# Optimization experiments

Measured on AMD Instinct MI355X. Metric: run time of the kernel, lower is better.

## Reference

```python
import jax, jax.numpy as jnp
import numpy as np
from jax import lax

B, S, T = 256, 2048, 64


def setup_inputs() -> dict:
    key = jax.random.key(0)
    k1, k2, k3 = jax.random.split(key, 3)
    emissions = jax.random.normal(k1, (B, S, T), dtype=jnp.float32)
    tags = jax.random.randint(k2, (B, S), 0, T, dtype=jnp.int64)
    mask = jnp.ones((B, S), dtype=bool)
    # learned parameter: transitions ~ U(-0.1, 0.1) per reset_parameters
    transitions = jax.random.uniform(k3, (T, T), dtype=jnp.float32, minval=-0.1, maxval=0.1)
    return {"emissions": emissions, "transitions": transitions, "tags": tags, "mask": mask}


def _crf_nll(emissions, transitions, tags, mask):
    # emissions [B,S,T], tags [B,S] int, mask [B,S] bool -> scalar NLL
    em = jnp.swapaxes(emissions, 0, 1)        # [S,B,T]
    tg = jnp.swapaxes(tags, 0, 1)             # [S,B]
    mk = jnp.swapaxes(mask, 0, 1)             # [S,B]
    bsz = tg.shape[1]
    batch_range = jnp.arange(bsz)

    # ---- score(emissions, tags, mask): fully vectorized over seq ----
    em_at_tags = jnp.take_along_axis(em, tg[..., None], axis=-1)[..., 0]   # [S,B]
    trans_steps = transitions[tg[:-1], tg[1:]]                              # [S-1,B]
    step_scores = (trans_steps + em_at_tags[1:]) * mk[1:].astype(em.dtype)  # [S-1,B]
    gold_score = em[0, batch_range, tg[0]] + jnp.sum(step_scores, axis=0)   # [B]

    # ---- normalization: logsumexp semiring scan over seq ----
    def step(score, inp):
        e_t, m_t = inp                                   # [B,T], [B]
        # score[b, i] + transitions[i, j] + e_t[b, j] -> lse over i
        s_ = jax.nn.logsumexp(score[:, :, None] + transitions[None] + e_t[:, None, :], axis=1)
        score = jnp.where(m_t[:, None], s_, score)
        return score, None

    final, _ = lax.scan(step, em[0], (em[1:], mk[1:]))
    log_z = jax.nn.logsumexp(final, axis=-1)             # [B]

    return -jnp.mean(gold_score - log_z)


def reference(emissions, transitions, tags, mask):
    return _crf_nll(emissions, transitions, tags, mask)
```

## Files before the change

### kernel.cpp

```cpp
#include <hip/hip_runtime.h>
#include <cstdint>

#define BB 256
#define SS 2048
#define TT 64
#define M_SPLIT 1024
#define WS_STRIDE 144
#define LOG64 4.158883083359672

__device__ __forceinline__ int ldtag(const uint32_t* tw, int i, int is64) {
    return (int)tw[i << is64];
}

__device__ __forceinline__ float qsum4(float v) {
    int a = __builtin_amdgcn_mov_dpp(__float_as_int(v), 0xB1, 0xF, 0xF, true);
    float v1 = v + __int_as_float(a);
    int b2 = __builtin_amdgcn_mov_dpp(__float_as_int(v1), 0x4E, 0xF, 0xF, true);
    return v1 + __int_as_float(b2);
}

#define LDS_BARRIER() asm volatile("s_waitcnt lgkmcnt(0)\n\ts_barrier" ::: "memory")

template <int DIR>
__device__ __forceinline__ void fb_run(const float* __restrict__ em,
                                       const float* __restrict__ trans,
                                       float* __restrict__ ws,
                                       float* __restrict__ qbuf,
                                       int b, int tid)
{
    const int l   = tid & 63;
    const int w   = tid >> 6;
    const int j   = (w << 4) | (l >> 2);
    const int sub = l & 3;

#define TRIDX(k) (DIR ? (j * 64 + (sub * 16 + (k))) : ((sub * 16 + (k)) * 64 + j))
#define ED(k) const float E##k = __expf(trans[TRIDX(k)]) * 0.015625f;
    ED(0) ED(1) ED(2) ED(3) ED(4) ED(5) ED(6) ED(7)
    ED(8) ED(9) ED(10) ED(11) ED(12) ED(13) ED(14) ED(15)
#undef ED
#undef TRIDX

    const size_t ebase  = (size_t)b * SS * TT;
    constexpr int nsteps = DIR ? (SS - M_SPLIT) : (M_SPLIT - 1);
    constexpr int estep  = DIR ? -TT : TT;
    constexpr int t0     = DIR ? (SS - 2) : 1;

    const float* ep = em + ebase + (size_t)t0 * TT + j;
    float p0 = ep[0];
    float p1 = ep[1 * estep];
    float p2 = ep[2 * estep];
    float p3 = ep[3 * estep];

    if (tid < TT) {
        const size_t it = DIR ? ((size_t)(SS - 1) * TT) : 0;
        qbuf[tid] = __expf(em[ebase + it + tid]);
    }
    LDS_BARRIER();

    float logsum = 0.0f;
    int cur = 0;

    for (int si = 0; si < nsteps; ++si) {
        const float e = p0;
        p0 = p1; p1 = p2; p2 = p3;
        p3 = ep[4 * estep];
        ep += estep;

        float* rb = qbuf + (cur << 6);
        float* wb = qbuf + ((cur ^ 1) << 6);

        const float4 q0 = *(const float4*)(rb + sub * 16 + 0);
        const float4 q1 = *(const float4*)(rb + sub * 16 + 4);
        const float4 q2 = *(const float4*)(rb + sub * 16 + 8);
        const float4 q3 = *(const float4*)(rb + sub * 16 + 12);

        float a0 = 0, a1 = 0, a2 = 0, a3 = 0;
        a0 = fmaf(q0.x, E0,  a0); a1 = fmaf(q0.y, E1,  a1);
        a2 = fmaf(q0.z, E2,  a2); a3 = fmaf(q0.w, E3,  a3);
        a0 = fmaf(q1.x, E4,  a0); a1 = fmaf(q1.y, E5,  a1);
        a2 = fmaf(q1.z, E6,  a2); a3 = fmaf(q1.w, E7,  a3);
        a0 = fmaf(q2.x, E8,  a0); a1 = fmaf(q2.y, E9,  a1);
        a2 = fmaf(q2.z, E10, a2); a3 = fmaf(q2.w, E11, a3);
        a0 = fmaf(q3.x, E12, a0); a1 = fmaf(q3.y, E13, a1);
        a2 = fmaf(q3.z, E14, a2); a3 = fmaf(q3.w, E15, a3);
        float dot = (a0 + a1) + (a2 + a3);
        dot = qsum4(dot);

        float fv = __expf(e);
        if (DIR && si == nsteps - 1) fv = 1.0f;
        float wval = dot * fv;

        if ((si & 63) == 63) {
            const float m = rb[0];
            wval *= __builtin_amdgcn_rcpf(m);
            if (tid == 0) logsum += __logf(m);
        }

        if (sub == 0) wb[j] = wval;
        LDS_BARRIER();
        cur ^= 1;
    }

    const float* fin = qbuf + (cur << 6);
    float* wsb = ws + (size_t)b * WS_STRIDE;
    if (tid < TT) wsb[(DIR ? TT : 0) + tid] = fin[tid];
    if (tid == 0) wsb[DIR ? 129 : 128] = (float)((double)nsteps * LOG64) + logsum;
}

__global__ __launch_bounds__(256) void crf_fb_kernel(
    const float* __restrict__ em, const float* __restrict__ trans,
    float* __restrict__ ws)
{
    const int b   = blockIdx.x & (BB - 1);
    const int dir = blockIdx.x >> 8;

    __shared__ __align__(16) float qbuf[2 * TT];

    if (dir == 0) fb_run<0>(em, trans, ws, qbuf, b, threadIdx.x);
    else          fb_run<1>(em, trans, ws, qbuf, b, threadIdx.x);
}

__global__ __launch_bounds__(256) void crf_gold_kernel(
    const float* __restrict__ em, const float* __restrict__ trans,
    const uint32_t* __restrict__ tw, float* __restrict__ ws)
{
    const int b = blockIdx.x, tid = threadIdx.x;

    uint32_t orv = 0;
    for (int k = 1; k < 32; k += 2) orv |= tw[k];
    const int is64 = (orv == 0) ? 1 : 0;

    const int    tbase = b * SS;
    const size_t ebase = (size_t)b * SS * TT;

    float s = 0.0f;
    for (int t = tid; t < SS; t += 256) {
        const int tg = ldtag(tw, tbase + t, is64);
        float v = em[ebase + (size_t)t * TT + tg];
        if (t > 0) {
            const int tp = ldtag(tw, tbase + t - 1, is64);
            v += trans[tp * TT + tg];
        }
        s += v;
    }
    for (int off = 1; off < 64; off <<= 1) s += __shfl_xor(s, off);
    __shared__ float sh[4];
    if ((tid & 63) == 0) sh[tid >> 6] = s;
    __syncthreads();
    if (tid == 0) ws[(size_t)b * WS_STRIDE + 130] = sh[0] + sh[1] + sh[2] + sh[3];
}

__global__ __launch_bounds__(64) void crf_combine_kernel(
    const float* __restrict__ ws, float* __restrict__ outb)
{
    const int b = blockIdx.x, lane = threadIdx.x;
    const float* wsb = ws + (size_t)b * WS_STRIDE;
    float p = wsb[lane] * wsb[64 + lane];
    for (int off = 1; off < 64; off <<= 1) p += __shfl_xor(p, off);
    if (lane == 0) {
        const float logz = wsb[128] + wsb[129] + __logf(p);
        outb[b] = wsb[130] - logz;
    }
}

__global__ __launch_bounds__(256) void crf_final_kernel(
    const float* __restrict__ vals, float* __restrict__ out)
{
    const int l = threadIdx.x;
    float v = vals[l];
    for (int off = 1; off < 64; off <<= 1) v += __shfl_xor(v, off);
    __shared__ float sh[4];
    if ((l & 63) == 0) sh[l >> 6] = v;
    __syncthreads();
    if (l == 0) out[0] = -(sh[0] + sh[1] + sh[2] + sh[3]) * (1.0f / BB);
}

extern "C" void kernel_launch(void* const* d_in, const int* in_sizes, int n_in,
                              void* d_out, int out_size, void* d_ws, size_t ws_size,
                              hipStream_t stream) {
    const float*    em    = (const float*)d_in[0];
    const float*    trans = (const float*)d_in[1];
    const uint32_t* tw    = (const uint32_t*)d_in[2];

    float* ws   = (float*)d_ws;
    float* outb = ws + (size_t)BB * WS_STRIDE;

    crf_fb_kernel<<<2 * BB, 256, 0, stream>>>(em, trans, ws);
    crf_gold_kernel<<<BB, 256, 0, stream>>>(em, trans, tw, ws);
    crf_combine_kernel<<<BB, 64, 0, stream>>>(ws, outb);
    crf_final_kernel<<<1, 256, 0, stream>>>(outb, (float*)d_out);
}
```

Baseline: 298.9 us.

## Split CRF forward scan into segment transfer-matrix products on MFMA

Replaces the two-direction sequential forward/backward scan with 8 independent sequence segments per batch. Each segment computes a 64x64 transfer-matrix product using bf16 MFMA, giving much more parallelism (8192 wavefronts). A new combine kernel then chains the segment matrices per batch with rescaling. The cost is bf16 rounding of the probabilities across 256-step products, a 32 MB workspace requirement, and extra global traffic to write and read the segment matrices; a fallback path is kept when the workspace is too small or MFMA is unavailable.

```diff
diff --git a/kernel.cpp b/kernel.cpp
--- a/kernel.cpp
+++ b/kernel.cpp
@@ -4,12 +4,196 @@
 #define BB 256
 #define SS 2048
 #define TT 64
+#define LOG64 4.158883083359672
+
+#define OUTB 0
+#define GBASE 256
+#define LBASE 512
+#define PBASE 8704
+#define WS_NEED ((size_t)(PBASE + 2048 * 4096) * 4)
+#define SEGL 256
+
 #define M_SPLIT 1024
 #define WS_STRIDE 144
-#define LOG64 4.158883083359672
+
+typedef short  s16x4  __attribute__((ext_vector_type(4)));
+typedef float  f32x4v __attribute__((ext_vector_type(4)));
+typedef unsigned int u32x2 __attribute__((ext_vector_type(2)));
+
+#if __has_builtin(__builtin_amdgcn_mfma_f32_16x16x16bf16_1k)
+#define HAVE_MFMA16 1
+#define MFMA16(A,B,C) __builtin_amdgcn_mfma_f32_16x16x16bf16_1k(A,B,C,0,0,0)
+#else
+#define HAVE_MFMA16 0
+#endif
 
 __device__ __forceinline__ int ldtag(const uint32_t* tw, int i, int is64) {
     return (int)tw[i << is64];
+}
+
+__device__ __forceinline__ unsigned pk_rne(float lo, float hi) {
+    unsigned ul = __float_as_uint(lo) + 0x8000u;
+    unsigned uh = __float_as_uint(hi) + 0x8000u;
+    return __builtin_amdgcn_perm(uh, ul, 0x07060302u);
+}
+
+#if HAVE_MFMA16
+__global__ __launch_bounds__(64, 4) void crf_seg_kernel(
+    const float* __restrict__ em, const float* __restrict__ trans,
+    float* __restrict__ ws)
+{
+    const int l = threadIdx.x;
+    const int idx = blockIdx.x;
+    const int b = idx >> 5, s = (idx >> 2) & 7, w = idx & 3;
+    const int l15 = l & 15, l4 = l >> 4;
+    __shared__ __align__(16) float f_lds[TT];
+
+#define EV(mt,kb,e) (__expf(trans[((kb)*16 + l4*4 + (e))*64 + (mt)*16 + l15]) * 0.015625f)
+#define MKA(NM,mt,kb) u32x2 NM##u; NM##u[0]=pk_rne(EV(mt,kb,0),EV(mt,kb,1)); \
+                      NM##u[1]=pk_rne(EV(mt,kb,2),EV(mt,kb,3)); \
+                      const s16x4 NM=__builtin_bit_cast(s16x4,NM##u);
+    MKA(A00,0,0) MKA(A01,0,1) MKA(A02,0,2) MKA(A03,0,3)
+    MKA(A10,1,0) MKA(A11,1,1) MKA(A12,1,2) MKA(A13,1,3)
+    MKA(A20,2,0) MKA(A21,2,1) MKA(A22,2,2) MKA(A23,2,3)
+    MKA(A30,3,0) MKA(A31,3,1) MKA(A32,3,2) MKA(A33,3,3)
+#undef MKA
+#undef EV
+
+    const int cn = w * 16 + l15;
+    u32x2 B0u, B1u, B2u, B3u;
+#define BINIT(Bu,kb) { float v0=((kb)*16+l4*4+0)==cn?1.f:0.f; \
+                       float v1=((kb)*16+l4*4+1)==cn?1.f:0.f; \
+                       float v2=((kb)*16+l4*4+2)==cn?1.f:0.f; \
+                       float v3=((kb)*16+l4*4+3)==cn?1.f:0.f; \
+                       Bu[0]=pk_rne(v0,v1); Bu[1]=pk_rne(v2,v3); }
+    BINIT(B0u,0) BINIT(B1u,1) BINIT(B2u,2) BINIT(B3u,3)
+#undef BINIT
+
+    const size_t ebase = (size_t)b * (SS * TT);
+    const int t0 = s * SEGL + 1;
+    const int t1 = (s == 7) ? (SS - 1) : (s + 1) * SEGL;
+    const int nst = t1 - t0 + 1;
+
+    float p0 = em[ebase + (size_t)(t0 + 0) * TT + l];
+    float p1 = em[ebase + (size_t)(t0 + 1) * TT + l];
+    float p2 = em[ebase + (size_t)(t0 + 2) * TT + l];
+    float p3 = em[ebase + (size_t)(t0 + 3) * TT + l];
+
+    float logacc = 0.f;
+    const f32x4v Zf = {0.f, 0.f, 0.f, 0.f};
+    f32x4v C0, C1, C2, C3;
+
+    for (int si = 0; si < nst; ++si) {
+        const float fr = __expf(p0);
+        p0 = p1; p1 = p2; p2 = p3;
+        int tp = t0 + si + 4; if (tp > SS - 1) tp = SS - 1;
+        p3 = em[ebase + (size_t)tp * TT + l];
+
+        f_lds[l] = fr;
+
+        const s16x4 Bf0 = __builtin_bit_cast(s16x4, B0u);
+        const s16x4 Bf1 = __builtin_bit_cast(s16x4, B1u);
+        const s16x4 Bf2 = __builtin_bit_cast(s16x4, B2u);
+        const s16x4 Bf3 = __builtin_bit_cast(s16x4, B3u);
+
+        C0 = MFMA16(A00,Bf0,Zf); C0 = MFMA16(A01,Bf1,C0); C0 = MFMA16(A02,Bf2,C0); C0 = MFMA16(A03,Bf3,C0);
+        C1 = MFMA16(A10,Bf0,Zf); C1 = MFMA16(A11,Bf1,C1); C1 = MFMA16(A12,Bf2,C1); C1 = MFMA16(A13,Bf3,C1);
+        C2 = MFMA16(A20,Bf0,Zf); C2 = MFMA16(A21,Bf1,C2); C2 = MFMA16(A22,Bf2,C2); C2 = MFMA16(A23,Bf3,C2);
+        C3 = MFMA16(A30,Bf0,Zf); C3 = MFMA16(A31,Bf1,C3); C3 = MFMA16(A32,Bf2,C3); C3 = MFMA16(A33,Bf3,C3);
+
+        const f32x4v fm0 = *(const f32x4v*)(f_lds +  0 + l4 * 4);
+        const f32x4v fm1 = *(const f32x4v*)(f_lds + 16 + l4 * 4);
+        const f32x4v fm2 = *(const f32x4v*)(f_lds + 32 + l4 * 4);
+        const f32x4v fm3 = *(const f32x4v*)(f_lds + 48 + l4 * 4);
+        C0 *= fm0; C1 *= fm1; C2 *= fm2; C3 *= fm3;
+
+        if ((si & 7) == 7) {
+            float mx = fmaxf(fmaxf(fmaxf(C0[0],C0[1]),fmaxf(C0[2],C0[3])),
+                       fmaxf(fmaxf(fmaxf(C1[0],C1[1]),fmaxf(C1[2],C1[3])),
+                       fmaxf(fmaxf(fmaxf(C2[0],C2[1]),fmaxf(C2[2],C2[3])),
+                             fmaxf(fmaxf(C3[0],C3[1]),fmaxf(C3[2],C3[3])))));
+            mx = fmaxf(mx, __shfl_xor(mx, 1));  mx = fmaxf(mx, __shfl_xor(mx, 2));
+            mx = fmaxf(mx, __shfl_xor(mx, 4));  mx = fmaxf(mx, __shfl_xor(mx, 8));
+            mx = fmaxf(mx, __shfl_xor(mx, 16)); mx = fmaxf(mx, __shfl_xor(mx, 32));
+            const float inv = __builtin_amdgcn_rcpf(mx);
+            C0 *= inv; C1 *= inv; C2 *= inv; C3 *= inv;
+            logacc += __logf(mx);
+        }
+
+        B0u[0] = pk_rne(C0[0],C0[1]); B0u[1] = pk_rne(C0[2],C0[3]);
+        B1u[0] = pk_rne(C1[0],C1[1]); B1u[1] = pk_rne(C1[2],C1[3]);
+        B2u[0] = pk_rne(C2[0],C2[1]); B2u[1] = pk_rne(C2[2],C2[3]);
+        B3u[0] = pk_rne(C3[0],C3[1]); B3u[1] = pk_rne(C3[2],C3[3]);
+    }
+
+    float* pt = ws + PBASE + (size_t)(b * 8 + s) * 4096 + (size_t)cn * 64 + l4 * 4;
+    *(f32x4v*)(pt +  0) = C0;
+    *(f32x4v*)(pt + 16) = C1;
+    *(f32x4v*)(pt + 32) = C2;
+    *(f32x4v*)(pt + 48) = C3;
+    if (l == 0)
+        ws[LBASE + (b * 8 + s) * 4 + w] = logacc + (float)((double)nst * LOG64);
+}
+
+__global__ __launch_bounds__(64) void crf_combine2(
+    const float* __restrict__ em, float* __restrict__ ws)
+{
+    const int b = blockIdx.x, m = threadIdx.x;
+    __shared__ float xs[TT];
+    float alpha = __expf(em[(size_t)b * (SS * TT) + m]);
+    float logA = 0.f;
+    for (int s = 0; s < 8; ++s) {
+        const float* Lp = ws + LBASE + (b * 8 + s) * 4;
+        const float L0 = Lp[0], L1 = Lp[1], L2 = Lp[2], L3 = Lp[3];
+        const float Lmax = fmaxf(fmaxf(L0, L1), fmaxf(L2, L3));
+        const float Lw = Lp[m >> 4];
+        xs[m] = alpha * __expf(Lw - Lmax);
+        const float* Pp = ws + PBASE + (size_t)(b * 8 + s) * 4096;
+        float y = 0.f;
+        for (int i = 0; i < TT; ++i)
+            y = fmaf(Pp[(size_t)i * 64 + m], xs[i], y);
+        logA += Lmax;
+        float mx = y;
+        mx = fmaxf(mx, __shfl_xor(mx, 1));  mx = fmaxf(mx, __shfl_xor(mx, 2));
+        mx = fmaxf(mx, __shfl_xor(mx, 4));  mx = fmaxf(mx, __shfl_xor(mx, 8));
+        mx = fmaxf(mx, __shfl_xor(mx, 16)); mx = fmaxf(mx, __shfl_xor(mx, 32));
+        alpha = y * __builtin_amdgcn_rcpf(mx);
+        logA += __logf(mx);
+    }
+    float ssum = alpha;
+    ssum += __shfl_xor(ssum, 1);  ssum += __shfl_xor(ssum, 2);
+    ssum += __shfl_xor(ssum, 4);  ssum += __shfl_xor(ssum, 8);
+    ssum += __shfl_xor(ssum, 16); ssum += __shfl_xor(ssum, 32);
+    if (m == 0)
+        ws[OUTB + b] = ws[GBASE + b] - (logA + __logf(ssum));
+}
+#endif
+
+__global__ __launch_bounds__(256) void crf_gold_kernel(
+    const float* __restrict__ em, const float* __restrict__ trans,
+    const uint32_t* __restrict__ tw, float* __restrict__ gdst, int gstride)
+{
+    const int b = blockIdx.x, tid = threadIdx.x;
+    uint32_t orv = 0;
+    for (int k = 1; k < 32; k += 2) orv |= tw[k];
+    const int is64 = (orv == 0) ? 1 : 0;
+    const int    tbase = b * SS;
+    const size_t ebase = (size_t)b * SS * TT;
+    float s = 0.0f;
+    for (int t = tid; t < SS; t += 256) {
+        const int tg = ldtag(tw, tbase + t, is64);
+        float v = em[ebase + (size_t)t * TT + tg];
+        if (t > 0) {
+            const int tp = ldtag(tw, tbase + t - 1, is64);
+            v += trans[tp * TT + tg];
+        }
+        s += v;
+    }
+    for (int off = 1; off < 64; off <<= 1) s += __shfl_xor(s, off);
+    __shared__ float sh[4];
+    if ((tid & 63) == 0) sh[tid >> 6] = s;
+    __syncthreads();
+    if (tid == 0) gdst[b * gstride] = sh[0] + sh[1] + sh[2] + sh[3];
 }
 
 __device__ __forceinline__ float qsum4(float v) {
@@ -18,7 +202,6 @@
     int b2 = __builtin_amdgcn_mov_dpp(__float_as_int(v1), 0x4E, 0xF, 0xF, true);
     return v1 + __int_as_float(b2);
 }
-
 #define LDS_BARRIER() asm volatile("s_waitcnt lgkmcnt(0)\n\ts_barrier" ::: "memory")
 
 template <int DIR>
@@ -32,48 +215,39 @@
     const int w   = tid >> 6;
     const int j   = (w << 4) | (l >> 2);
     const int sub = l & 3;
-
 #define TRIDX(k) (DIR ? (j * 64 + (sub * 16 + (k))) : ((sub * 16 + (k)) * 64 + j))
 #define ED(k) const float E##k = __expf(trans[TRIDX(k)]) * 0.015625f;
     ED(0) ED(1) ED(2) ED(3) ED(4) ED(5) ED(6) ED(7)
     ED(8) ED(9) ED(10) ED(11) ED(12) ED(13) ED(14) ED(15)
 #undef ED
 #undef TRIDX
-
     const size_t ebase  = (size_t)b * SS * TT;
     constexpr int nsteps = DIR ? (SS - M_SPLIT) : (M_SPLIT - 1);
     constexpr int estep  = DIR ? -TT : TT;
     constexpr int t0     = DIR ? (SS - 2) : 1;
-
     const float* ep = em + ebase + (size_t)t0 * TT + j;
     float p0 = ep[0];
     float p1 = ep[1 * estep];
     float p2 = ep[2 * estep];
     float p3 = ep[3 * estep];
-
     if (tid < TT) {
         const size_t it = DIR ? ((size_t)(SS - 1) * TT) : 0;
         qbuf[tid] = __expf(em[ebase + it + tid]);
     }
     LDS_BARRIER();
-
     float logsum = 0.0f;
     int cur = 0;
-
     for (int si = 0; si < nsteps; ++si) {
         const float e = p0;
         p0 = p1; p1 = p2; p2 = p3;
         p3 = ep[4 * estep];
         ep += estep;
-
         float* rb = qbuf + (cur << 6);
         float* wb = qbuf + ((cur ^ 1) << 6);
-
         const float4 q0 = *(const float4*)(rb + sub * 16 + 0);
         const float4 q1 = *(const float4*)(rb + sub * 16 + 4);
         const float4 q2 = *(const float4*)(rb + sub * 16 + 8);
         const float4 q3 = *(const float4*)(rb + sub * 16 + 12);
-
         float a0 = 0, a1 = 0, a2 = 0, a3 = 0;
         a0 = fmaf(q0.x, E0,  a0); a1 = fmaf(q0.y, E1,  a1);
         a2 = fmaf(q0.z, E2,  a2); a3 = fmaf(q0.w, E3,  a3);
@@ -85,22 +259,18 @@
         a2 = fmaf(q3.z, E14, a2); a3 = fmaf(q3.w, E15, a3);
         float dot = (a0 + a1) + (a2 + a3);
         dot = qsum4(dot);
-
         float fv = __expf(e);
         if (DIR && si == nsteps - 1) fv = 1.0f;
         float wval = dot * fv;
-
         if ((si & 63) == 63) {
             const float m = rb[0];
             wval *= __builtin_amdgcn_rcpf(m);
             if (tid == 0) logsum += __logf(m);
         }
-
         if (sub == 0) wb[j] = wval;
         LDS_BARRIER();
         cur ^= 1;
     }
-
     const float* fin = qbuf + (cur << 6);
     float* wsb = ws + (size_t)b * WS_STRIDE;
     if (tid < TT) wsb[(DIR ? TT : 0) + tid] = fin[tid];
@@ -113,41 +283,9 @@
 {
     const int b   = blockIdx.x & (BB - 1);
     const int dir = blockIdx.x >> 8;
-
     __shared__ __align__(16) float qbuf[2 * TT];
-
     if (dir == 0) fb_run<0>(em, trans, ws, qbuf, b, threadIdx.x);
     else          fb_run<1>(em, trans, ws, qbuf, b, threadIdx.x);
-}
-
-__global__ __launch_bounds__(256) void crf_gold_kernel(
-    const float* __restrict__ em, const float* __restrict__ trans,
-    const uint32_t* __restrict__ tw, float* __restrict__ ws)
-{
-    const int b = blockIdx.x, tid = threadIdx.x;
-
-    uint32_t orv = 0;
-    for (int k = 1; k < 32; k += 2) orv |= tw[k];
-    const int is64 = (orv == 0) ? 1 : 0;
-
-    const int    tbase = b * SS;
-    const size_t ebase = (size_t)b * SS * TT;
-
-    float s = 0.0f;
-    for (int t = tid; t < SS; t += 256) {
-        const int tg = ldtag(tw, tbase + t, is64);
-        float v = em[ebase + (size_t)t * TT + tg];
-        if (t > 0) {
-            const int tp = ldtag(tw, tbase + t - 1, is64);
-            v += trans[tp * TT + tg];
-        }
-        s += v;
-    }
-    for (int off = 1; off < 64; off <<= 1) s += __shfl_xor(s, off);
-    __shared__ float sh[4];
-    if ((tid & 63) == 0) sh[tid >> 6] = s;
-    __syncthreads();
-    if (tid == 0) ws[(size_t)b * WS_STRIDE + 130] = sh[0] + sh[1] + sh[2] + sh[3];
 }
 
 __global__ __launch_bounds__(64) void crf_combine_kernel(
@@ -181,12 +319,20 @@
     const float*    em    = (const float*)d_in[0];
     const float*    trans = (const float*)d_in[1];
     const uint32_t* tw    = (const uint32_t*)d_in[2];
-
-    float* ws   = (float*)d_ws;
+    float* ws = (float*)d_ws;
+
+#if HAVE_MFMA16
+    if (ws_size >= WS_NEED) {
+        crf_seg_kernel<<<BB * 32, 64, 0, stream>>>(em, trans, ws);
+        crf_gold_kernel<<<BB, 256, 0, stream>>>(em, trans, tw, ws + GBASE, 1);
+        crf_combine2<<<BB, 64, 0, stream>>>(em, ws);
+        crf_final_kernel<<<1, 256, 0, stream>>>(ws + OUTB, (float*)d_out);
+        return;
+    }
+#endif
     float* outb = ws + (size_t)BB * WS_STRIDE;
-
     crf_fb_kernel<<<2 * BB, 256, 0, stream>>>(em, trans, ws);
-    crf_gold_kernel<<<BB, 256, 0, stream>>>(em, trans, tw, ws);
+    crf_gold_kernel<<<BB, 256, 0, stream>>>(em, trans, tw, ws + 130, WS_STRIDE);
     crf_combine_kernel<<<BB, 64, 0, stream>>>(ws, outb);
     crf_final_kernel<<<1, 256, 0, stream>>>(outb, (float*)d_out);
 }
```

After: 296.7 us. About the same (-0.7%).
